# Optimization experiments

Measured on AMD Instinct MI355X. Metric: run time of the kernel, lower is better.

Reference implementation:

```python
import jax, jax.numpy as jnp
import numpy as np

N, DIM, T_ITERS = 8192, 64, 4

def setup_inputs() -> dict:
    key = jax.random.key(0)
    ks = jax.random.split(key, 9)
    graph = jax.random.normal(ks[0], (N, N), jnp.float32)
    x = jax.random.randint(ks[1], (N,), 0, 2, jnp.int32)  # 0/1 indicator of S
    theta1 = jax.random.normal(ks[2], (1, DIM), jnp.float32)
    theta2 = jax.random.normal(ks[3], (DIM, DIM), jnp.float32)
    theta3 = jax.random.normal(ks[4], (DIM, DIM), jnp.float32)
    theta4 = jax.random.normal(ks[5], (1, DIM), jnp.float32)
    theta5 = jax.random.normal(ks[6], (2 * DIM, 1), jnp.float32)
    theta6 = jax.random.normal(ks[7], (DIM, DIM), jnp.float32)
    theta7 = jax.random.normal(ks[8], (DIM, DIM), jnp.float32)
    return dict(graph=graph, x=x, theta1=theta1, theta2=theta2, theta3=theta3,
                theta4=theta4, theta5=theta5, theta6=theta6, theta7=theta7,
                v=100, T=T_ITERS)


def reference(graph, x, theta1, theta2, theta3, theta4, theta5, theta6, theta7, v, T):
    dt = graph.dtype
    xf = x.astype(dt)  # (N,)
    # c_v = sum_u relu(theta4 * graph[v,u]) @ theta3.
    # Exact identity: relu(t*w) = max(w,0)*relu(t) + max(-w,0)*relu(-t),
    s_pos = jnp.maximum(graph, 0.0).sum(axis=1)   # (N,)
    s_neg = jnp.maximum(-graph, 0.0).sum(axis=1)  # (N,)
    t4 = theta4[0]  # (dim,)
    c = (s_pos[:, None] * jax.nn.relu(t4)
         + s_neg[:, None] * jax.nn.relu(-t4)) @ theta3  # (N, dim)
    a = xf[:, None] * theta1  # (N, dim) via broadcast of (1, dim)

    def step(u, _):
        summ = u.sum(axis=0, keepdims=True)        # (1, dim)
        b = (summ - u) @ theta2                    # (N, dim)
        return jax.nn.relu(a + b + c), None

    u0 = jnp.zeros((graph.shape[0], theta1.shape[1]), dt)
    u, _ = jax.lax.scan(step, u0, None, length=T)

    summ = u.sum(axis=0)                           # (dim,)
    q_in = jnp.concatenate([summ @ theta6, u[v] @ theta7])  # (2*dim,)
    return jax.nn.relu(q_in) @ theta5              # (1,)
```

## Files before the change

kernel.cpp:

```cpp
#include <hip/hip_runtime.h>
#include <hip/hip_bf16.h>

#define NN 8192
#define DIM 64
#define T_IT 4

__global__ __launch_bounds__(256) void rowsum_kernel(
    const float* __restrict__ graph,
    float* __restrict__ s_pos, float* __restrict__ s_neg) {
  const int row = blockIdx.x;
  const int t = threadIdx.x;
  const float4* g = (const float4*)(graph + (size_t)row * NN);
  float sp = 0.f, sn = 0.f;
#pragma unroll
  for (int it = 0; it < NN / 4 / 256; ++it) {
    float4 v = g[t + it * 256];
    sp += fmaxf(v.x, 0.f) + fmaxf(v.y, 0.f) + fmaxf(v.z, 0.f) + fmaxf(v.w, 0.f);
    sn += fmaxf(-v.x, 0.f) + fmaxf(-v.y, 0.f) + fmaxf(-v.z, 0.f) + fmaxf(-v.w, 0.f);
  }
  for (int off = 32; off > 0; off >>= 1) {
    sp += __shfl_down(sp, off);
    sn += __shfl_down(sn, off);
  }
  __shared__ float lds[2][4];
  const int wave = t >> 6;
  if ((t & 63) == 0) { lds[0][wave] = sp; lds[1][wave] = sn; }
  __syncthreads();
  if (t == 0) {
    s_pos[row] = lds[0][0] + lds[0][1] + lds[0][2] + lds[0][3];
    s_neg[row] = lds[1][0] + lds[1][1] + lds[1][2] + lds[1][3];
  }
}

__global__ void prep_kernel(const float* __restrict__ theta3,
                            const float* __restrict__ theta4,
                            float* __restrict__ pq) {
  const int d = threadIdx.x;
  float p = 0.f, q = 0.f;
  for (int k = 0; k < DIM; ++k) {
    const float t4 = theta4[k];
    const float th = theta3[k * DIM + d];
    p += fmaxf(t4, 0.f) * th;
    q += fmaxf(-t4, 0.f) * th;
  }
  pq[d] = p;
  pq[DIM + d] = q;
}

__global__ __launch_bounds__(256) void update_kernel(
    const float* __restrict__ theta1, const float* __restrict__ theta2,
    const int* __restrict__ x, const float* __restrict__ s_pos,
    const float* __restrict__ s_neg, const float* __restrict__ pq,
    const float* __restrict__ summ_in, float* __restrict__ summ_out,
    float* __restrict__ u) {
  __shared__ float th2[DIM * DIM];
  __shared__ float gsh[DIM];
  __shared__ float ush[4][DIM];
  __shared__ float red[4][DIM];
  const int t = threadIdx.x;
  const int d = t & 63;
  const int r = t >> 6;

  for (int i = t; i < DIM * DIM; i += 256) th2[i] = theta2[i];
  __syncthreads();
  if (t < DIM) {
    float g = 0.f;
    for (int k = 0; k < DIM; ++k) g += summ_in[k] * th2[k * DIM + d];
    gsh[d] = g;
  }
  const float pd = pq[d];
  const float qd = pq[DIM + d];
  const float t1d = theta1[d];
  __syncthreads();
  const float gd = gsh[d];

  float acc = 0.f;
  for (int base = blockIdx.x * 4; base < NN; base += gridDim.x * 4) {
    const int row = base + r;
    ush[r][d] = u[(size_t)row * DIM + d];
    __syncthreads();
    float dot = 0.f;
#pragma unroll
    for (int k = 0; k < DIM; ++k) dot += ush[r][k] * th2[k * DIM + d];
    float val = (float)x[row] * t1d + s_pos[row] * pd + s_neg[row] * qd + gd - dot;
    val = fmaxf(val, 0.f);
    u[(size_t)row * DIM + d] = val;
    acc += val;
    __syncthreads();
  }
  red[r][d] = acc;
  __syncthreads();
  if (r == 0) {
    const float s = red[0][d] + red[1][d] + red[2][d] + red[3][d];
    atomicAdd(&summ_out[d], s);
  }
}

__global__ void final_kernel(const float* __restrict__ theta5,
                             const float* __restrict__ theta6,
                             const float* __restrict__ theta7,
                             const float* __restrict__ summ,
                             const float* __restrict__ u,
                             const int* __restrict__ vptr,
                             float* __restrict__ out) {
  const int t = threadIdx.x;
  const int d = t & 63;
  float h;
  if (t < DIM) {
    float s = 0.f;
    for (int k = 0; k < DIM; ++k) s += summ[k] * theta6[k * DIM + d];
    h = fmaxf(s, 0.f) * theta5[d];
  } else {
    const int v = *vptr;
    const float* uv = u + (size_t)v * DIM;
    float s = 0.f;
    for (int k = 0; k < DIM; ++k) s += uv[k] * theta7[k * DIM + d];
    h = fmaxf(s, 0.f) * theta5[DIM + d];
  }
  __shared__ float red[128];
  red[t] = h;
  __syncthreads();
  if (t == 0) {
    float s = 0.f;
    for (int i = 0; i < 128; ++i) s += red[i];
    out[0] = s;
  }
}

extern "C" void kernel_launch(void* const* d_in, const int* in_sizes, int n_in,
                              void* d_out, int out_size, void* d_ws, size_t ws_size,
                              hipStream_t stream) {
  const float* graph  = (const float*)d_in[0];
  const int*   x      = (const int*)d_in[1];
  const float* theta1 = (const float*)d_in[2];
  const float* theta2 = (const float*)d_in[3];
  const float* theta3 = (const float*)d_in[4];
  const float* theta4 = (const float*)d_in[5];
  const float* theta5 = (const float*)d_in[6];
  const float* theta6 = (const float*)d_in[7];
  const float* theta7 = (const float*)d_in[8];
  const int*   vptr   = (const int*)d_in[9];
  float* out = (float*)d_out;

  float* ws    = (float*)d_ws;
  float* s_pos = ws;
  float* s_neg = ws + NN;
  float* pq    = ws + 2 * NN;
  float* summ  = ws + 2 * NN + 128;
  float* u     = ws + 2 * NN + 448;

  const size_t zero_off_bytes = (size_t)(2 * NN + 128) * sizeof(float);
  const size_t zero_len_bytes = (size_t)(320 + (size_t)NN * DIM) * sizeof(float);
  hipMemsetAsync((char*)d_ws + zero_off_bytes, 0, zero_len_bytes, stream);

  rowsum_kernel<<<NN, 256, 0, stream>>>(graph, s_pos, s_neg);
  prep_kernel<<<1, DIM, 0, stream>>>(theta3, theta4, pq);
  for (int t = 0; t < T_IT; ++t) {
    update_kernel<<<256, 256, 0, stream>>>(theta1, theta2, x, s_pos, s_neg, pq,
                                           summ + t * DIM, summ + (t + 1) * DIM, u);
  }
  final_kernel<<<1, 128, 0, stream>>>(theta5, theta6, theta7,
                                      summ + T_IT * DIM, u, vptr, out);
}
```

Before: 448.6 us.

## Fuse row-sum pass with first iteration and drop the workspace memset

Computes the graph row sums one wave per row and directly produces the first iteration's u (u0=0, so the theta2 term vanishes), removing one step kernel launch. Zeroing of the summ buffers moves into prep_kernel, which replaces the large memset of u. The inner theta2 dot product now reads u from shared memory as float4. The fused kernel runs 512 blocks of 4 waves, each wave handling a full 32KB row with its own reduction. That gives different occupancy and memory-level parallelism than the old one-block-per-row layout.

```diff
diff --git a/kernel.cpp b/kernel.cpp
--- a/kernel.cpp
+++ b/kernel.cpp
@@ -1,40 +1,13 @@
 #include <hip/hip_runtime.h>
-#include <hip/hip_bf16.h>
 
 #define NN 8192
 #define DIM 64
 #define T_IT 4
 
-__global__ __launch_bounds__(256) void rowsum_kernel(
-    const float* __restrict__ graph,
-    float* __restrict__ s_pos, float* __restrict__ s_neg) {
-  const int row = blockIdx.x;
-  const int t = threadIdx.x;
-  const float4* g = (const float4*)(graph + (size_t)row * NN);
-  float sp = 0.f, sn = 0.f;
-#pragma unroll
-  for (int it = 0; it < NN / 4 / 256; ++it) {
-    float4 v = g[t + it * 256];
-    sp += fmaxf(v.x, 0.f) + fmaxf(v.y, 0.f) + fmaxf(v.z, 0.f) + fmaxf(v.w, 0.f);
-    sn += fmaxf(-v.x, 0.f) + fmaxf(-v.y, 0.f) + fmaxf(-v.z, 0.f) + fmaxf(-v.w, 0.f);
-  }
-  for (int off = 32; off > 0; off >>= 1) {
-    sp += __shfl_down(sp, off);
-    sn += __shfl_down(sn, off);
-  }
-  __shared__ float lds[2][4];
-  const int wave = t >> 6;
-  if ((t & 63) == 0) { lds[0][wave] = sp; lds[1][wave] = sn; }
-  __syncthreads();
-  if (t == 0) {
-    s_pos[row] = lds[0][0] + lds[0][1] + lds[0][2] + lds[0][3];
-    s_neg[row] = lds[1][0] + lds[1][1] + lds[1][2] + lds[1][3];
-  }
-}
-
 __global__ void prep_kernel(const float* __restrict__ theta3,
                             const float* __restrict__ theta4,
-                            float* __restrict__ pq) {
+                            float* __restrict__ pq,
+                            float* __restrict__ summ) {
   const int d = threadIdx.x;
   float p = 0.f, q = 0.f;
   for (int k = 0; k < DIM; ++k) {
@@ -45,9 +18,59 @@
   }
   pq[d] = p;
   pq[DIM + d] = q;
+#pragma unroll
+  for (int t = 0; t < T_IT; ++t) summ[t * DIM + d] = 0.f;
 }
 
-__global__ __launch_bounds__(256) void update_kernel(
+__global__ __launch_bounds__(256) void fused_rowsum_step1(
+    const float* __restrict__ graph, const int* __restrict__ x,
+    const float* __restrict__ theta1, const float* __restrict__ pq,
+    float* __restrict__ s_pos, float* __restrict__ s_neg,
+    float* __restrict__ u, float* __restrict__ summ1) {
+  const int wave = threadIdx.x >> 6;
+  const int lane = threadIdx.x & 63;
+  const float pd = pq[lane];
+  const float qd = pq[DIM + lane];
+  const float t1d = theta1[lane];
+  float accd = 0.f;
+
+  for (int row = blockIdx.x * 4 + wave; row < NN; row += 2048) {
+    const float4* g = (const float4*)(graph + (size_t)row * NN);
+    float sp = 0.f, sn = 0.f;
+    for (int it = 0; it < NN / 4 / 64; it += 8) {
+#pragma unroll
+      for (int j = 0; j < 8; ++j) {
+        const float4 v = g[lane + (it + j) * 64];
+        sp += fmaxf(v.x, 0.f) + fmaxf(v.y, 0.f) + fmaxf(v.z, 0.f) + fmaxf(v.w, 0.f);
+        sn += fmaxf(-v.x, 0.f) + fmaxf(-v.y, 0.f) + fmaxf(-v.z, 0.f) + fmaxf(-v.w, 0.f);
+      }
+    }
+#pragma unroll
+    for (int off = 32; off > 0; off >>= 1) {
+      sp += __shfl_down(sp, off);
+      sn += __shfl_down(sn, off);
+    }
+    sp = __shfl(sp, 0);
+    sn = __shfl(sn, 0);
+    if (lane == 0) {
+      s_pos[row] = sp;
+      s_neg[row] = sn;
+    }
+    const float acv = (float)x[row] * t1d + sp * pd + sn * qd;
+    const float uv = fmaxf(acv, 0.f);
+    u[(size_t)row * DIM + lane] = uv;
+    accd += uv;
+  }
+
+  __shared__ float red[4][DIM];
+  red[wave][lane] = accd;
+  __syncthreads();
+  if (wave == 0)
+    atomicAdd(&summ1[lane],
+              red[0][lane] + red[1][lane] + red[2][lane] + red[3][lane]);
+}
+
+__global__ __launch_bounds__(256) void step_kernel(
     const float* __restrict__ theta1, const float* __restrict__ theta2,
     const int* __restrict__ x, const float* __restrict__ s_pos,
     const float* __restrict__ s_neg, const float* __restrict__ pq,
@@ -55,7 +78,7 @@
     float* __restrict__ u) {
   __shared__ float th2[DIM * DIM];
   __shared__ float gsh[DIM];
-  __shared__ float ush[4][DIM];
+  __shared__ __align__(16) float ush[4][DIM];
   __shared__ float red[4][DIM];
   const int t = threadIdx.x;
   const int d = t & 63;
@@ -80,10 +103,17 @@
     ush[r][d] = u[(size_t)row * DIM + d];
     __syncthreads();
     float dot = 0.f;
+    const float4* ur = (const float4*)ush[r];
 #pragma unroll
-    for (int k = 0; k < DIM; ++k) dot += ush[r][k] * th2[k * DIM + d];
-    float val = (float)x[row] * t1d + s_pos[row] * pd + s_neg[row] * qd + gd - dot;
-    val = fmaxf(val, 0.f);
+    for (int kk = 0; kk < DIM / 4; ++kk) {
+      const float4 uv = ur[kk];
+      dot += uv.x * th2[(4 * kk + 0) * DIM + d];
+      dot += uv.y * th2[(4 * kk + 1) * DIM + d];
+      dot += uv.z * th2[(4 * kk + 2) * DIM + d];
+      dot += uv.w * th2[(4 * kk + 3) * DIM + d];
+    }
+    const float acv = (float)x[row] * t1d + s_pos[row] * pd + s_neg[row] * qd;
+    float val = fmaxf(acv + gd - dot, 0.f);
     u[(size_t)row * DIM + d] = val;
     acc += val;
     __syncthreads();
@@ -91,8 +121,7 @@
   red[r][d] = acc;
   __syncthreads();
   if (r == 0) {
-    const float s = red[0][d] + red[1][d] + red[2][d] + red[3][d];
-    atomicAdd(&summ_out[d], s);
+    atomicAdd(&summ_out[d], red[0][d] + red[1][d] + red[2][d] + red[3][d]);
   }
 }
 
@@ -143,22 +172,19 @@
   float* out = (float*)d_out;
 
   float* ws    = (float*)d_ws;
-  float* s_pos = ws;
-  float* s_neg = ws + NN;
-  float* pq    = ws + 2 * NN;
-  float* summ  = ws + 2 * NN + 128;
-  float* u     = ws + 2 * NN + 448;
+  float* pq    = ws;
+  float* summ  = ws + 128;
+  float* s_pos = ws + 128 + T_IT * DIM;
+  float* s_neg = s_pos + NN;
+  float* u     = s_neg + NN;
 
-  const size_t zero_off_bytes = (size_t)(2 * NN + 128) * sizeof(float);
-  const size_t zero_len_bytes = (size_t)(320 + (size_t)NN * DIM) * sizeof(float);
-  hipMemsetAsync((char*)d_ws + zero_off_bytes, 0, zero_len_bytes, stream);
-
-  rowsum_kernel<<<NN, 256, 0, stream>>>(graph, s_pos, s_neg);
-  prep_kernel<<<1, DIM, 0, stream>>>(theta3, theta4, pq);
-  for (int t = 0; t < T_IT; ++t) {
-    update_kernel<<<256, 256, 0, stream>>>(theta1, theta2, x, s_pos, s_neg, pq,
-                                           summ + t * DIM, summ + (t + 1) * DIM, u);
+  prep_kernel<<<1, DIM, 0, stream>>>(theta3, theta4, pq, summ);
+  fused_rowsum_step1<<<512, 256, 0, stream>>>(graph, x, theta1, pq,
+                                              s_pos, s_neg, u, summ);
+  for (int t = 1; t < T_IT; ++t) {
+    step_kernel<<<256, 256, 0, stream>>>(theta1, theta2, x, s_pos, s_neg, pq,
+                                         summ + (t - 1) * DIM, summ + t * DIM, u);
   }
   final_kernel<<<1, 128, 0, stream>>>(theta5, theta6, theta7,
-                                      summ + T_IT * DIM, u, vptr, out);
+                                      summ + (T_IT - 1) * DIM, u, vptr, out);
 }
```

Measured after the change: 431.3 us. -3.9%, faster.
